# Kernel tuning notes

Measured on AMD Instinct MI355X. Metric: run time of the kernel, lower is better.

The kernel has to match this reference:

```python
import jax, jax.numpy as jnp
import numpy as np

EMBED_DIM = 1024
NUM_HEADS = 16
HEAD_DIM = EMBED_DIM // NUM_HEADS


def setup_inputs() -> dict:
    key = jax.random.key(0)
    k_x, k_wqkv, k_bqkv, k_wout, k_bout = jax.random.split(key, 5)
    B, T, C = 4, 2048, EMBED_DIM
    bound_qkv = 1.0 / np.sqrt(C)
    bound_out = 1.0 / np.sqrt(C)
    return {
        "x": jax.random.normal(k_x, (B, T, C), dtype=jnp.float32),
        # nn.Linear stores weight as [out, in]; we keep that convention.
        "w_qkv": jax.random.uniform(k_wqkv, (3 * C, C), jnp.float32, -bound_qkv, bound_qkv),
        "b_qkv": jax.random.uniform(k_bqkv, (3 * C,), jnp.float32, -bound_qkv, bound_qkv),
        "w_out": jax.random.uniform(k_wout, (C, C), jnp.float32, -bound_out, bound_out),
        "b_out": jax.random.uniform(k_bout, (C,), jnp.float32, -bound_out, bound_out),
    }


def reference(x, w_qkv, b_qkv, w_out, b_out):
    B, T, C = x.shape
    H, D = NUM_HEADS, HEAD_DIM
    qkv = x @ w_qkv.T + b_qkv                     # [B, T, 3C]
    qkv = qkv.reshape(B, T, 3, H, D)
    q = jnp.transpose(qkv[:, :, 0], (0, 2, 1, 3))  # [B, H, T, D]
    k = jnp.transpose(qkv[:, :, 1], (0, 2, 1, 3))
    v = jnp.transpose(qkv[:, :, 2], (0, 2, 1, 3))
    att = jnp.einsum('bhqd,bhkd->bhqk', q, k) / jnp.sqrt(jnp.float32(D))
    causal = jnp.tril(jnp.ones((T, T), dtype=bool))
    att = jnp.where(causal[None, None], att, -jnp.inf)
    att = jax.nn.softmax(att, axis=-1)
    # dropout p=0.0 (eval-mode identity)
    out = jnp.einsum('bhqk,bhkd->bhqd', att, v)    # [B, H, T, D]
    out = jnp.transpose(out, (0, 2, 1, 3)).reshape(B, T, C)
    return out @ w_out.T + b_out
```

## Files before the change

### kernel.cpp

```cpp
#include <hip/hip_runtime.h>
#include <hip/hip_bf16.h>


#define B_ 4
#define T_ 2048
#define C_ 1024
#define H_ 16
#define D_ 64
#define M_ (B_*T_)

#define SCALE_LOG2 0.18033688f

typedef __attribute__((ext_vector_type(8))) short short8;
typedef __attribute__((ext_vector_type(4))) float f32x4;
typedef __attribute__((ext_vector_type(16))) float f32x16;

static __device__ __forceinline__ ushort f2bf(float f) {
  __hip_bfloat16 b = __float2bfloat16(f);
  ushort u; __builtin_memcpy(&u, &b, 2); return u;
}

static __device__ __forceinline__ void ld16(const void* g, void* l) {
  __builtin_amdgcn_global_load_lds((const __attribute__((address_space(1))) void*)g,
                                   (__attribute__((address_space(3))) void*)l, 16, 0, 0);
}

static __device__ __forceinline__ f32x4 mfma16(short8 a, short8 b, f32x4 c) {
  return __builtin_amdgcn_mfma_f32_16x16x32_bf16(a, b, c, 0, 0, 0);
}
static __device__ __forceinline__ f32x16 mfma32(short8 a, short8 b, f32x16 c) {
  return __builtin_amdgcn_mfma_f32_32x32x16_bf16(a, b, c, 0, 0, 0);
}

static __device__ __forceinline__ float pair_max(float x) {
  return fmaxf(x, __shfl_xor(x, 32));
}
static __device__ __forceinline__ float pair_sum(float x) {
  return x + __shfl_xor(x, 32);
}

__global__ void cvt3(const float* __restrict__ a, const float* __restrict__ b,
                     const float* __restrict__ c, ushort* __restrict__ oa,
                     ushort* __restrict__ ob, ushort* __restrict__ oc,
                     int na, int nb, int nc) {
  int tot = na + nb + nc;
  int i = blockIdx.x * blockDim.x + threadIdx.x;
  int st = gridDim.x * blockDim.x;
  for (; i < tot; i += st) {
    const float* s; ushort* d; int k = i;
    if (k < na)            { s = a; d = oa; }
    else if (k < na + nb)  { k -= na; s = b; d = ob; }
    else                   { k -= na + nb; s = c; d = oc; }
    float4 v = ((const float4*)s)[k];
    ushort4 o;
    o.x = f2bf(v.x); o.y = f2bf(v.y); o.z = f2bf(v.z); o.w = f2bf(v.w);
    ((ushort4*)d)[k] = o;
  }
}

template<int MODE>
__global__ __launch_bounds__(256) void gemm_bt(
    const ushort* __restrict__ A, const ushort* __restrict__ Bm,
    const float* __restrict__ bias, int K,
    ushort* __restrict__ q, ushort* __restrict__ kk, ushort* __restrict__ vt,
    float* __restrict__ outF)
{
  __shared__ ushort SM[17408];
  const int tid = threadIdx.x;
  const int lane = tid & 63;
  const int w = tid >> 6;
  const int wr = w >> 1, wc = w & 1;
  const int l15 = lane & 15, lhi = lane >> 4;
  const long i0 = (long)blockIdx.y * 128;
  const long j0 = (long)blockIdx.x * 128;

  const int gsw = (lhi ^ ((l15 >> 1) & 3)) * 8;

  auto STAGE = [&](int buf, int k0) {
    int c = tid;
    int row = c >> 2, gs = (c & 3) ^ ((row >> 1) & 3);
    ld16((const char*)A  + ((i0 + row) * K + k0 + gs * 8) * 2, (char*)SM + buf*8192 + c*16);
    ld16((const char*)Bm + ((j0 + row) * K + k0 + gs * 8) * 2, (char*)SM + 16384 + buf*8192 + c*16);
    c = tid + 256;
    row = c >> 2; gs = (c & 3) ^ ((row >> 1) & 3);
    ld16((const char*)A  + ((i0 + row) * K + k0 + gs * 8) * 2, (char*)SM + buf*8192 + c*16);
    ld16((const char*)Bm + ((j0 + row) * K + k0 + gs * 8) * 2, (char*)SM + 16384 + buf*8192 + c*16);
  };

  f32x4 acc[4][4] = {};
  const int nsteps = K >> 5;

  STAGE(0, 0);
  STAGE(1, 32);
  int cur = 0;

  for (int t = 0; t < nsteps; t++) {
    if (t + 1 < nsteps) { asm volatile("s_waitcnt vmcnt(4)" ::: "memory"); }
    else                { asm volatile("s_waitcnt vmcnt(0)" ::: "memory"); }
    __builtin_amdgcn_s_barrier();
    __builtin_amdgcn_sched_barrier(0);

    short8 af[4], bf[4];
#pragma unroll
    for (int m = 0; m < 4; m++)
      af[m] = *(const short8*)&SM[cur*4096 + (wr*64 + m*16 + l15)*32 + gsw];
#pragma unroll
    for (int n = 0; n < 4; n++)
      bf[n] = *(const short8*)&SM[8192 + cur*4096 + (wc*64 + n*16 + l15)*32 + gsw];
    __builtin_amdgcn_s_setprio(1);
#pragma unroll
    for (int m = 0; m < 4; m++)
#pragma unroll
      for (int n = 0; n < 4; n++)
        acc[m][n] = mfma16(af[m], bf[n], acc[m][n]);
    __builtin_amdgcn_s_setprio(0);

    __builtin_amdgcn_s_barrier();
    __builtin_amdgcn_sched_barrier(0);
    if (t + 2 < nsteps) STAGE(cur, (t + 2) * 32);
    cur ^= 1;
  }

  if (MODE == 0 && j0 >= 2048) {
#pragma unroll
    for (int m = 0; m < 4; m++)
#pragma unroll
      for (int n = 0; n < 4; n++) {
        const int jl = wc*64 + n*16 + l15;
        const int tl = wr*64 + m*16 + lhi*4;
        const float bs = bias[j0 + jl];
        uint w0, w1;
        asm("v_cvt_pk_bf16_f32 %0, %1, %2" : "=v"(w0)
            : "v"(acc[m][n][0] + bs), "v"(acc[m][n][1] + bs));
        asm("v_cvt_pk_bf16_f32 %0, %1, %2" : "=v"(w1)
            : "v"(acc[m][n][2] + bs), "v"(acc[m][n][3] + bs));
        uint2 pr; pr.x = w0; pr.y = w1;
        *(uint2*)&SM[jl * 136 + tl] = pr;
      }
    __syncthreads();
    const int b = (int)(i0 >> 11);
    const int tb = (int)(i0 & 2047);
#pragma unroll
    for (int k2 = 0; k2 < 8; k2++) {
      const int chunk = k2 * 256 + tid;
      const int jl = chunk >> 4;
      const int t0 = (chunk & 15) * 8;
      uint4 pw = *(const uint4*)&SM[jl * 136 + t0];
      const int cc = (int)((j0 + jl) & 1023);
      const int h = cc >> 6, d = cc & 63;
      *(uint4*)&vt[((size_t)(b * H_ + h) * D_ + d) * T_ + tb + t0] = pw;
    }
  } else {
#pragma unroll
    for (int m = 0; m < 4; m++) {
#pragma unroll
      for (int n = 0; n < 4; n++) {
#pragma unroll
        for (int r = 0; r < 4; r++) {
          long i = i0 + wr*64 + m*16 + lhi*4 + r;
          int  j = (int)j0 + wc*64 + n*16 + l15;
          float v = acc[m][n][r] + bias[j];
          if (MODE == 0) {
            int b = (int)(i >> 11), t = (int)(i & 2047);
            int cc = j & 1023;
            int h = cc >> 6, d = cc & 63;
            long bh = (long)b * H_ + h;
            if (j < 1024)      q [(bh*T_ + t)*D_ + d] = f2bf(v * SCALE_LOG2);
            else               kk[(bh*T_ + t)*D_ + d] = f2bf(v);
          } else {
            outF[i * C_ + j] = v;
          }
        }
      }
    }
  }
}

#define PSTR 20

static __device__ __forceinline__ void softmax_pack32(
    f32x16& sc, float& m, float& lp, f32x16 (&o)[2],
    int q0, int kvbase, int l31, int hi, uint* __restrict__ P)
{
  float sv[16];
  const bool needmask = (kvbase + 31 > q0);
#pragma unroll
  for (int r = 0; r < 16; r++) {
    float xv = sc[r];
    if (needmask) {
      int kv = kvbase + (r & 3) + 8 * (r >> 2) + 4 * hi;
      if (kv > q0 + l31) xv = -1e30f;
    }
    sv[r] = xv;
  }
  float p0 = fmaxf(fmaxf(sv[0], sv[1]),  fmaxf(sv[2], sv[3]));
  float p1 = fmaxf(fmaxf(sv[4], sv[5]),  fmaxf(sv[6], sv[7]));
  float p2 = fmaxf(fmaxf(sv[8], sv[9]),  fmaxf(sv[10], sv[11]));
  float p3 = fmaxf(fmaxf(sv[12], sv[13]), fmaxf(sv[14], sv[15]));
  float pm = fmaxf(fmaxf(p0, p1), fmaxf(p2, p3));
  float rowm = pair_max(pm);
  float nm = fmaxf(m, rowm);
  float alpha = __builtin_amdgcn_exp2f(m - nm);
  m = nm;
  lp *= alpha;
#pragma unroll
  for (int dt = 0; dt < 2; dt++)
#pragma unroll
    for (int r = 0; r < 16; r++) o[dt][r] *= alpha;
  float s = 0.f;
#pragma unroll
  for (int r = 0; r < 16; r++) {
    float p = __builtin_amdgcn_exp2f(sv[r] - m);
    sv[r] = p;
    s += p;
  }
  lp += s;
  uint W[8];
#pragma unroll
  for (int r = 0; r < 8; r++)
    asm("v_cvt_pk_bf16_f32 %0, %1, %2" : "=v"(W[r]) : "v"(sv[2*r]), "v"(sv[2*r+1]));
#pragma unroll
  for (int r2 = 0; r2 < 4; r2++) {
    uint2 pr; pr.x = W[2*r2]; pr.y = W[2*r2 + 1];
    *(uint2*)&P[l31 * PSTR + r2*4 + 2*hi] = pr;
  }
}

__global__ __launch_bounds__(256, 2) void attn_k(
    const ushort* __restrict__ Q, const ushort* __restrict__ K,
    const ushort* __restrict__ V, ushort* __restrict__ AO)
{
  __shared__ ushort Kt[2][128*64];
  __shared__ ushort Vt[2][64*128];
  __shared__ uint P2[4][32 * PSTR];
  const int tid = threadIdx.x;
  const int lane = tid & 63;
  const int w = tid >> 6;
  const int l31 = lane & 31, hi = lane >> 5;
  const int bb = blockIdx.x;
  const int head = bb & 63;
  const int rblk = 15 - (bb >> 6);
  const int nst = rblk + 1;
  const int q0 = 128 * rblk + 32 * w;

  const ushort* Qb = Q + (size_t)head * T_ * D_;
  const ushort* Kb = K + (size_t)head * T_ * D_;
  const ushort* Vb = V + (size_t)head * D_ * T_;

  auto STAGE = [&](int buf, int kv0s) {
#pragma unroll
    for (int hb = 0; hb < 4; hb++) {
      int slot = tid + hb * 256;
      int krow = slot >> 3, kg = slot & 7, kgs = kg ^ (krow & 7);
      ld16((const char*)Kb + ((size_t)(kv0s + krow) * D_ + kgs * 8) * 2,
           (char*)&Kt[buf][0] + slot * 16);
      int vrow = slot >> 4, vg = slot & 15, vgs = vg ^ (vrow & 15);
      ld16((const char*)Vb + ((size_t)vrow * T_ + kv0s + vgs * 8) * 2,
           (char*)&Vt[buf][0] + slot * 16);
    }
  };

  short8 qf[4];
#pragma unroll
  for (int s = 0; s < 4; s++)
    qf[s] = *(const short8*)&Qb[(q0 + l31) * D_ + s*16 + hi*8];

  f32x16 o[2] = {};
  float m = -1e30f, lp = 0.f;

  STAGE(0, 0);
  STAGE(1, 128);
  int cur = 0;
  uint* P = &P2[w][0];

  for (int t = 0; t < nst; t++) {
    const int kv0 = t * 128;
    if (t + 1 < nst) { asm volatile("s_waitcnt vmcnt(8)" ::: "memory"); }
    else             { asm volatile("s_waitcnt vmcnt(0)" ::: "memory"); }
    __builtin_amdgcn_s_barrier();
    __builtin_amdgcn_sched_barrier(0);

#pragma unroll
    for (int c = 0; c < 4; c++) {
      const int kvc = kv0 + 32 * c;
      if (kvc <= q0 + 31) {
        short8 kf[4];
#pragma unroll
        for (int s = 0; s < 4; s++) {
          const int row = c*32 + l31;
          kf[s] = *(const short8*)&Kt[cur][row*64 + (((2*s + hi) ^ (row & 7)) << 3)];
        }
        short8 vf[2][2];
#pragma unroll
        for (int sl = 0; sl < 2; sl++)
#pragma unroll
          for (int dt = 0; dt < 2; dt++) {
            const int row = dt*32 + l31;
            const int u = c*4 + sl*2 + hi;
            vf[sl][dt] = *(const short8*)
                &Vt[cur][row*128 + ((u ^ (row & 15)) << 3)];
          }

        f32x16 sc = {};
        __builtin_amdgcn_s_setprio(1);
#pragma unroll
        for (int s = 0; s < 4; s++) sc = mfma32(kf[s], qf[s], sc);
        __builtin_amdgcn_s_setprio(0);
        softmax_pack32(sc, m, lp, o, q0, kvc, l31, hi, P);
        asm volatile("s_waitcnt lgkmcnt(0)" ::: "memory");
        __builtin_amdgcn_sched_barrier(0);
        short8 pf[2];
#pragma unroll
        for (int sl = 0; sl < 2; sl++) {
          uint4 pw = *(const uint4*)&P[l31 * PSTR + sl*8 + hi*4];
          __builtin_memcpy(&pf[sl], &pw, 16);
        }
        __builtin_amdgcn_s_setprio(1);
#pragma unroll
        for (int sl = 0; sl < 2; sl++)
#pragma unroll
          for (int dt = 0; dt < 2; dt++)
            o[dt] = mfma32(vf[sl][dt], pf[sl], o[dt]);
        __builtin_amdgcn_s_setprio(0);
        __builtin_amdgcn_sched_barrier(0);
      }
    }

    __builtin_amdgcn_s_barrier();
    __builtin_amdgcn_sched_barrier(0);
    if (t + 2 < nst) STAGE(cur, kv0 + 256);
    cur ^= 1;
  }

  const int b = head >> 4, h = head & 15;
  const float invl = 1.0f / pair_sum(lp);
  const size_t rowb = (size_t)(b * T_ + q0 + l31) * C_ + h * 64;
#pragma unroll
  for (int dt = 0; dt < 2; dt++)
#pragma unroll
    for (int rg = 0; rg < 4; rg++) {
      const int d0 = dt*32 + 8*rg + 4*hi;
      ushort4 ov;
      ov.x = f2bf(o[dt][rg*4+0] * invl);
      ov.y = f2bf(o[dt][rg*4+1] * invl);
      ov.z = f2bf(o[dt][rg*4+2] * invl);
      ov.w = f2bf(o[dt][rg*4+3] * invl);
      *(ushort4*)&AO[rowb + d0] = ov;
    }
}

extern "C" void kernel_launch(void* const* d_in, const int* in_sizes, int n_in,
                              void* d_out, int out_size, void* d_ws, size_t ws_size,
                              hipStream_t stream) {
  const float* x     = (const float*)d_in[0];
  const float* w_qkv = (const float*)d_in[1];
  const float* b_qkv = (const float*)d_in[2];
  const float* w_out = (const float*)d_in[3];
  const float* b_out = (const float*)d_in[4];
  float* out = (float*)d_out;

  ushort* xb    = (ushort*)d_ws;
  ushort* wqkvb = xb    + (size_t)M_ * C_;
  ushort* woutb = wqkvb + (size_t)3 * C_ * C_;
  ushort* q     = woutb + (size_t)C_ * C_;
  ushort* kk    = q     + (size_t)M_ * C_;
  ushort* vt    = kk    + (size_t)M_ * C_;
  ushort* ao    = xb;

  cvt3<<<2048, 256, 0, stream>>>(x, w_qkv, w_out, xb, wqkvb, woutb,
                                 (M_ * C_) / 4, (3 * C_ * C_) / 4, (C_ * C_) / 4);

  gemm_bt<0><<<dim3(3 * C_ / 128, M_ / 128), 256, 0, stream>>>(
      xb, wqkvb, b_qkv, C_, q, kk, vt, nullptr);

  attn_k<<<B_ * H_ * T_ / 128, 256, 0, stream>>>(q, kk, vt, ao);

  gemm_bt<1><<<dim3(C_ / 128, M_ / 128), 256, 0, stream>>>(
      ao, woutb, b_out, C_, nullptr, nullptr, nullptr, out);
}
```

Before: 184.6 us.

## Halve KV tile, raise occupancy, add lazy softmax rescale, drop waits

Result: faster. 169.2 us (-8.4%).

```diff
diff --git a/kernel.cpp b/kernel.cpp
--- a/kernel.cpp
+++ b/kernel.cpp
@@ -193,20 +193,23 @@
     }
     sv[r] = xv;
   }
-  float p0 = fmaxf(fmaxf(sv[0], sv[1]),  fmaxf(sv[2], sv[3]));
-  float p1 = fmaxf(fmaxf(sv[4], sv[5]),  fmaxf(sv[6], sv[7]));
-  float p2 = fmaxf(fmaxf(sv[8], sv[9]),  fmaxf(sv[10], sv[11]));
-  float p3 = fmaxf(fmaxf(sv[12], sv[13]), fmaxf(sv[14], sv[15]));
-  float pm = fmaxf(fmaxf(p0, p1), fmaxf(p2, p3));
-  float rowm = pair_max(pm);
-  float nm = fmaxf(m, rowm);
-  float alpha = __builtin_amdgcn_exp2f(m - nm);
-  m = nm;
-  lp *= alpha;
-#pragma unroll
-  for (int dt = 0; dt < 2; dt++)
-#pragma unroll
-    for (int r = 0; r < 16; r++) o[dt][r] *= alpha;
+  float a0 = fmaxf(fmaxf(sv[0], sv[1]), sv[2]);
+  float a1 = fmaxf(fmaxf(sv[3], sv[4]), sv[5]);
+  float a2 = fmaxf(fmaxf(sv[6], sv[7]), sv[8]);
+  float a3 = fmaxf(fmaxf(sv[9], sv[10]), sv[11]);
+  float a4 = fmaxf(fmaxf(sv[12], sv[13]), sv[14]);
+  float pmax = fmaxf(fmaxf(fmaxf(a0, a1), a2), fmaxf(fmaxf(a3, a4), sv[15]));
+  if (__any(pmax > m + 8.0f)) {
+    float rowm = pair_max(pmax);
+    float nm = fmaxf(m, rowm);
+    float alpha = __builtin_amdgcn_exp2f(m - nm);
+    m = nm;
+    lp *= alpha;
+#pragma unroll
+    for (int dt = 0; dt < 2; dt++)
+#pragma unroll
+      for (int r = 0; r < 16; r++) o[dt][r] *= alpha;
+  }
   float s = 0.f;
 #pragma unroll
   for (int r = 0; r < 16; r++) {
@@ -226,12 +229,12 @@
   }
 }
 
-__global__ __launch_bounds__(256, 2) void attn_k(
+__global__ __launch_bounds__(256, 3) void attn_k(
     const ushort* __restrict__ Q, const ushort* __restrict__ K,
     const ushort* __restrict__ V, ushort* __restrict__ AO)
 {
-  __shared__ ushort Kt[2][128*64];
-  __shared__ ushort Vt[2][64*128];
+  __shared__ ushort Kt[2][64*64];
+  __shared__ ushort Vt[2][64*64];
   __shared__ uint P2[4][32 * PSTR];
   const int tid = threadIdx.x;
   const int lane = tid & 63;
@@ -240,7 +243,7 @@
   const int bb = blockIdx.x;
   const int head = bb & 63;
   const int rblk = 15 - (bb >> 6);
-  const int nst = rblk + 1;
+  const int nst = 2 * rblk + 2;
   const int q0 = 128 * rblk + 32 * w;
 
   const ushort* Qb = Q + (size_t)head * T_ * D_;
@@ -249,13 +252,12 @@
 
   auto STAGE = [&](int buf, int kv0s) {
 #pragma unroll
-    for (int hb = 0; hb < 4; hb++) {
+    for (int hb = 0; hb < 2; hb++) {
       int slot = tid + hb * 256;
-      int krow = slot >> 3, kg = slot & 7, kgs = kg ^ (krow & 7);
-      ld16((const char*)Kb + ((size_t)(kv0s + krow) * D_ + kgs * 8) * 2,
+      int row = slot >> 3, g = slot & 7, gs = g ^ (row & 7);
+      ld16((const char*)Kb + ((size_t)(kv0s + row) * D_ + gs * 8) * 2,
            (char*)&Kt[buf][0] + slot * 16);
-      int vrow = slot >> 4, vg = slot & 15, vgs = vg ^ (vrow & 15);
-      ld16((const char*)Vb + ((size_t)vrow * T_ + kv0s + vgs * 8) * 2,
+      ld16((const char*)Vb + ((size_t)row * T_ + kv0s + gs * 8) * 2,
            (char*)&Vt[buf][0] + slot * 16);
     }
   };
@@ -269,19 +271,19 @@
   float m = -1e30f, lp = 0.f;
 
   STAGE(0, 0);
-  STAGE(1, 128);
+  STAGE(1, 64);
   int cur = 0;
   uint* P = &P2[w][0];
 
   for (int t = 0; t < nst; t++) {
-    const int kv0 = t * 128;
-    if (t + 1 < nst) { asm volatile("s_waitcnt vmcnt(8)" ::: "memory"); }
+    const int kv0 = t * 64;
+    if (t + 1 < nst) { asm volatile("s_waitcnt vmcnt(4)" ::: "memory"); }
     else             { asm volatile("s_waitcnt vmcnt(0)" ::: "memory"); }
     __builtin_amdgcn_s_barrier();
     __builtin_amdgcn_sched_barrier(0);
 
 #pragma unroll
-    for (int c = 0; c < 4; c++) {
+    for (int c = 0; c < 2; c++) {
       const int kvc = kv0 + 32 * c;
       if (kvc <= q0 + 31) {
         short8 kf[4];
@@ -297,8 +299,7 @@
           for (int dt = 0; dt < 2; dt++) {
             const int row = dt*32 + l31;
             const int u = c*4 + sl*2 + hi;
-            vf[sl][dt] = *(const short8*)
-                &Vt[cur][row*128 + ((u ^ (row & 15)) << 3)];
+            vf[sl][dt] = *(const short8*)&Vt[cur][row*64 + ((u ^ (row & 7)) << 3)];
           }
 
         f32x16 sc = {};
@@ -306,9 +307,8 @@
 #pragma unroll
         for (int s = 0; s < 4; s++) sc = mfma32(kf[s], qf[s], sc);
         __builtin_amdgcn_s_setprio(0);
+
         softmax_pack32(sc, m, lp, o, q0, kvc, l31, hi, P);
-        asm volatile("s_waitcnt lgkmcnt(0)" ::: "memory");
-        __builtin_amdgcn_sched_barrier(0);
         short8 pf[2];
 #pragma unroll
         for (int sl = 0; sl < 2; sl++) {
@@ -317,18 +317,17 @@
         }
         __builtin_amdgcn_s_setprio(1);
 #pragma unroll
-        for (int sl = 0; sl < 2; sl++)
-#pragma unroll
-          for (int dt = 0; dt < 2; dt++)
-            o[dt] = mfma32(vf[sl][dt], pf[sl], o[dt]);
+        for (int dt = 0; dt < 2; dt++) {
+          o[dt] = mfma32(vf[0][dt], pf[0], o[dt]);
+          o[dt] = mfma32(vf[1][dt], pf[1], o[dt]);
+        }
         __builtin_amdgcn_s_setprio(0);
-        __builtin_amdgcn_sched_barrier(0);
       }
     }
 
     __builtin_amdgcn_s_barrier();
     __builtin_amdgcn_sched_barrier(0);
-    if (t + 2 < nst) STAGE(cur, kv0 + 256);
+    if (t + 2 < nst) STAGE(cur, kv0 + 128);
     cur ^= 1;
   }
 
```
